# Performance work log

Hardware: AMD Instinct MI355X
Metric: run time of the kernel (lower is better)

Reference implementation:

```python
import jax, jax.numpy as jnp
import numpy as np

HIDDEN = 2048
INPUT = 2048
BATCH = 4096


def setup_inputs() -> dict:
    key = jax.random.key(0)
    ks = jax.random.split(key, 7)
    x = jax.random.normal(ks[0], (BATCH, INPUT), dtype=jnp.float32)
    h = jax.random.normal(ks[1], (BATCH, HIDDEN), dtype=jnp.float32)
    c = jax.random.normal(ks[2], (BATCH, HIDDEN), dtype=jnp.float32)
    # learned parameters (RandomNormal init stddev=0.05 analogue; scale irrelevant for correctness)
    w_ih = jax.random.normal(ks[3], (4, INPUT, HIDDEN), dtype=jnp.float32) * 0.05
    w_hh = jax.random.normal(ks[4], (4, HIDDEN, HIDDEN), dtype=jnp.float32) * 0.05
    b_ih = jax.random.normal(ks[5], (4, HIDDEN), dtype=jnp.float32) * 0.05
    b_hh = jax.random.normal(ks[6], (4, HIDDEN), dtype=jnp.float32) * 0.05
    return {"x": x, "h": h, "c": c, "w_ih": w_ih, "w_hh": w_hh, "b_ih": b_ih, "b_hh": b_hh}


def reference(x, h, c, w_ih, w_hh, b_ih, b_hh):
    # gates: [4, B, H] = x @ w_ih[g] and h @ w_hh[g], batched over gate dim g
    gates = (
        jnp.einsum("bi,gih->gbh", x, w_ih)
        + jnp.einsum("bh,ghk->gbk", h, w_hh)
        + (b_ih + b_hh)[:, None, :]
    )
    ingate = jax.nn.sigmoid(gates[0])
    forgetgate = jax.nn.sigmoid(gates[1])
    cellgate = jnp.tanh(gates[2])
    outgate = jax.nn.sigmoid(gates[3])
    c_new = forgetgate * c + ingate * cellgate
    h_new = outgate * jnp.tanh(c_new)
    return (h_new, c_new)
```

## Files before the change

kernel.cpp:

```cpp
#include <hip/hip_runtime.h>

#define BATCH  4096
#define HIDDEN 2048
#define INPUT  2048
#define KDIM   4096
#define NDIM   8192

#define BM 128
#define BN 128
#define BK 32

typedef __attribute__((ext_vector_type(8))) short short8;
typedef __attribute__((ext_vector_type(4))) float float4v;


__device__ __forceinline__ unsigned short f2bf(float f) {
    union { float f; unsigned u; } v; v.f = f;
    unsigned r = v.u + 0x7FFFu + ((v.u >> 16) & 1u);
    return (unsigned short)(r >> 16);
}

__device__ __forceinline__ void gl2lds16(const unsigned short* g, unsigned short* l) {
    __builtin_amdgcn_global_load_lds(
        (const __attribute__((address_space(1))) unsigned int*)g,
        (__attribute__((address_space(3))) unsigned int*)l,
        16, 0, 0);
}

__device__ __forceinline__ float sigm(float x) {
    return 1.0f / (1.0f + __expf(-x));
}
__device__ __forceinline__ float tanh_fast(float x) {
    return 2.0f / (1.0f + __expf(-2.0f * x)) - 1.0f;
}


__global__ void pack_x_kernel(const float* __restrict__ x, const float* __restrict__ h,
                              unsigned short* __restrict__ Xb) {
    int idx = blockIdx.x * 256 + threadIdx.x;
    int b  = idx >> 9;
    int ko = idx & 511;
    const float* src = (ko < 256) ? (x + (size_t)b * INPUT  + (size_t)ko * 8)
                                  : (h + (size_t)b * HIDDEN + (size_t)(ko - 256) * 8);
    float4 v0 = *(const float4*)(src);
    float4 v1 = *(const float4*)(src + 4);
    union { unsigned short us[8]; uint4 v; } o;
    o.us[0] = f2bf(v0.x); o.us[1] = f2bf(v0.y); o.us[2] = f2bf(v0.z); o.us[3] = f2bf(v0.w);
    o.us[4] = f2bf(v1.x); o.us[5] = f2bf(v1.y); o.us[6] = f2bf(v1.z); o.us[7] = f2bf(v1.w);
    *(uint4*)(Xb + (size_t)b * KDIM + (size_t)ko * 8) = o.v;
}


__global__ void pack_w_kernel(const float* __restrict__ w_ih, const float* __restrict__ w_hh,
                              unsigned short* __restrict__ Wt) {
    __shared__ float tile[64][33];
    int k0 = blockIdx.x * 64;
    int n0 = blockIdx.y * 32;
    int g  = n0 >> 11;
    int j0 = n0 & 2047;
    const float* src = (k0 < INPUT)
        ? (w_ih + (size_t)g * INPUT  * HIDDEN + (size_t)k0 * HIDDEN + j0)
        : (w_hh + (size_t)g * HIDDEN * HIDDEN + (size_t)(k0 - INPUT) * HIDDEN + j0);

    int tcol = threadIdx.x & 31;
    int trow = threadIdx.x >> 5;
#pragma unroll
    for (int p = 0; p < 8; ++p)
        tile[trow + p * 8][tcol] = src[(size_t)(trow + p * 8) * HIDDEN + tcol];
    __syncthreads();

    int tk = threadIdx.x & 63;
    int tn = threadIdx.x >> 6;
#pragma unroll
    for (int p = 0; p < 8; ++p)
        Wt[(size_t)(n0 + tn + p * 4) * KDIM + k0 + tk] = f2bf(tile[tk][tn + p * 4]);
}


__global__ __launch_bounds__(256, 2)
void gemm_kernel(const unsigned short* __restrict__ A,
                 const unsigned short* __restrict__ B,
                 float* __restrict__ C) {
    __shared__ unsigned short As[BM * BK];
    __shared__ unsigned short Bs[BN * BK];

    const int tid  = threadIdx.x;
    const int m0   = blockIdx.y * BM;
    const int n0   = blockIdx.x * BN;
    const int wave = tid >> 6;
    const int lane = tid & 63;
    const int ln   = lane & 15;
    const int kq   = lane >> 4;
    const int wm   = (wave >> 1) * 64;
    const int wn   = (wave & 1) * 64;

    const int s0 = tid, s1 = tid + 256;
    const unsigned short* gA0 = A + (size_t)(m0 + (s0 >> 2)) * KDIM + (s0 & 3) * 8;
    const unsigned short* gA1 = A + (size_t)(m0 + (s1 >> 2)) * KDIM + (s1 & 3) * 8;
    const unsigned short* gB0 = B + (size_t)(n0 + (s0 >> 2)) * KDIM + (s0 & 3) * 8;
    const unsigned short* gB1 = B + (size_t)(n0 + (s1 >> 2)) * KDIM + (s1 & 3) * 8;
    unsigned short* lA0 = As + s0 * 8;
    unsigned short* lA1 = As + s1 * 8;
    unsigned short* lB0 = Bs + s0 * 8;
    unsigned short* lB1 = Bs + s1 * 8;

    float4v acc[4][4];
#pragma unroll
    for (int i = 0; i < 4; ++i)
#pragma unroll
        for (int j = 0; j < 4; ++j)
            acc[i][j] = (float4v){0.f, 0.f, 0.f, 0.f};

    const int a_off = (wm + ln) * BK + kq * 8;
    const int b_off = (wn + ln) * BK + kq * 8;

    for (int kt = 0; kt < KDIM / BK; ++kt) {
        const int ko = kt * BK;
        gl2lds16(gA0 + ko, lA0);
        gl2lds16(gA1 + ko, lA1);
        gl2lds16(gB0 + ko, lB0);
        gl2lds16(gB1 + ko, lB1);
        __syncthreads();

        short8 af[4], bf[4];
#pragma unroll
        for (int mi = 0; mi < 4; ++mi)
            af[mi] = *(const short8*)(As + a_off + mi * 16 * BK);
#pragma unroll
        for (int ni = 0; ni < 4; ++ni)
            bf[ni] = *(const short8*)(Bs + b_off + ni * 16 * BK);

#pragma unroll
        for (int mi = 0; mi < 4; ++mi)
#pragma unroll
            for (int ni = 0; ni < 4; ++ni)
                acc[mi][ni] = __builtin_amdgcn_mfma_f32_16x16x32_bf16(
                    af[mi], bf[ni], acc[mi][ni], 0, 0, 0);

        __syncthreads();
    }

#pragma unroll
    for (int mi = 0; mi < 4; ++mi) {
#pragma unroll
        for (int ni = 0; ni < 4; ++ni) {
            int col  = n0 + wn + ni * 16 + ln;
            int rowb = m0 + wm + mi * 16 + kq * 4;
#pragma unroll
            for (int j = 0; j < 4; ++j)
                C[(size_t)(rowb + j) * NDIM + col] = acc[mi][ni][j];
        }
    }
}


__global__ void lstm_epilogue_kernel(const float* __restrict__ Cg, const float* __restrict__ c,
                                     const float* __restrict__ b_ih, const float* __restrict__ b_hh,
                                     float* __restrict__ out) {
    int idx = blockIdx.x * 256 + threadIdx.x;
    int b = idx >> 9;
    int j = (idx & 511) * 4;

    const float* row = Cg + (size_t)b * NDIM;
    float4 g0 = *(const float4*)(row + j);
    float4 g1 = *(const float4*)(row + HIDDEN + j);
    float4 g2 = *(const float4*)(row + 2 * HIDDEN + j);
    float4 g3 = *(const float4*)(row + 3 * HIDDEN + j);

    float4 bi0 = *(const float4*)(b_ih + j);
    float4 bi1 = *(const float4*)(b_ih + HIDDEN + j);
    float4 bi2 = *(const float4*)(b_ih + 2 * HIDDEN + j);
    float4 bi3 = *(const float4*)(b_ih + 3 * HIDDEN + j);
    float4 bh0 = *(const float4*)(b_hh + j);
    float4 bh1 = *(const float4*)(b_hh + HIDDEN + j);
    float4 bh2 = *(const float4*)(b_hh + 2 * HIDDEN + j);
    float4 bh3 = *(const float4*)(b_hh + 3 * HIDDEN + j);

    float4 cv = *(const float4*)(c + (size_t)b * HIDDEN + j);

    float4 hn, cn;
    {
        float ig = sigm(g0.x + bi0.x + bh0.x);
        float fg = sigm(g1.x + bi1.x + bh1.x);
        float cg = tanh_fast(g2.x + bi2.x + bh2.x);
        float og = sigm(g3.x + bi3.x + bh3.x);
        cn.x = fg * cv.x + ig * cg;
        hn.x = og * tanh_fast(cn.x);
    }
    {
        float ig = sigm(g0.y + bi0.y + bh0.y);
        float fg = sigm(g1.y + bi1.y + bh1.y);
        float cg = tanh_fast(g2.y + bi2.y + bh2.y);
        float og = sigm(g3.y + bi3.y + bh3.y);
        cn.y = fg * cv.y + ig * cg;
        hn.y = og * tanh_fast(cn.y);
    }
    {
        float ig = sigm(g0.z + bi0.z + bh0.z);
        float fg = sigm(g1.z + bi1.z + bh1.z);
        float cg = tanh_fast(g2.z + bi2.z + bh2.z);
        float og = sigm(g3.z + bi3.z + bh3.z);
        cn.z = fg * cv.z + ig * cg;
        hn.z = og * tanh_fast(cn.z);
    }
    {
        float ig = sigm(g0.w + bi0.w + bh0.w);
        float fg = sigm(g1.w + bi1.w + bh1.w);
        float cg = tanh_fast(g2.w + bi2.w + bh2.w);
        float og = sigm(g3.w + bi3.w + bh3.w);
        cn.w = fg * cv.w + ig * cg;
        hn.w = og * tanh_fast(cn.w);
    }

    size_t o = (size_t)b * HIDDEN + j;
    *(float4*)(out + o) = hn;
    *(float4*)(out + (size_t)BATCH * HIDDEN + o) = cn;
}


extern "C" void kernel_launch(void* const* d_in, const int* in_sizes, int n_in,
                              void* d_out, int out_size, void* d_ws, size_t ws_size,
                              hipStream_t stream) {
    const float* x    = (const float*)d_in[0];
    const float* h    = (const float*)d_in[1];
    const float* c    = (const float*)d_in[2];
    const float* w_ih = (const float*)d_in[3];
    const float* w_hh = (const float*)d_in[4];
    const float* b_ih = (const float*)d_in[5];
    const float* b_hh = (const float*)d_in[6];
    float* out = (float*)d_out;

    const size_t XB_BYTES = (size_t)BATCH * KDIM * 2;
    const size_t WT_BYTES = (size_t)NDIM * KDIM * 2;
    unsigned short* Xb = (unsigned short*)d_ws;
    unsigned short* Wt = (unsigned short*)((char*)d_ws + XB_BYTES);
    float*          Cg = (float*)((char*)d_ws + XB_BYTES + WT_BYTES);

    hipLaunchKernelGGL(pack_x_kernel, dim3((size_t)BATCH * KDIM / 8 / 256), dim3(256), 0, stream,
                       x, h, Xb);
    hipLaunchKernelGGL(pack_w_kernel, dim3(KDIM / 64, NDIM / 32), dim3(256), 0, stream,
                       w_ih, w_hh, Wt);
    hipLaunchKernelGGL(gemm_kernel, dim3(NDIM / BN, BATCH / BM), dim3(256), 0, stream,
                       Xb, Wt, Cg);
    hipLaunchKernelGGL(lstm_epilogue_kernel, dim3((size_t)BATCH * HIDDEN / 4 / 256), dim3(256), 0, stream,
                       Cg, c, b_ih, b_hh, out);
}
```

Before: 590.6 us.

## Interleave gate columns in packed weights and fuse LSTM epilogue into GEMM

The weight pack now interleaves the four gate columns for each hidden unit (column 4*j+g), so each 16-column MFMA tile holds all four gates for four hidden units. The GEMM epilogue uses lane shuffles to bring the four gate values of one (row, hidden) pair into one lane, applies the bias and LSTM nonlinearities, and writes h_new and c_new directly. This removes the 128 MB fp32 gate intermediate write and read-back and one kernel launch. In exchange the output stores are scalar and strided rather than float4, and the epilogue does extra shuffles and per-lane loads of c and bias.

```diff
diff --git a/kernel.cpp b/kernel.cpp
--- a/kernel.cpp
+++ b/kernel.cpp
@@ -5,7 +5,6 @@
 #define INPUT  2048
 #define KDIM   4096
 #define NDIM   8192
-
 #define BM 128
 #define BN 128
 #define BK 32
@@ -72,15 +71,20 @@
     int tk = threadIdx.x & 63;
     int tn = threadIdx.x >> 6;
 #pragma unroll
-    for (int p = 0; p < 8; ++p)
-        Wt[(size_t)(n0 + tn + p * 4) * KDIM + k0 + tk] = f2bf(tile[tk][tn + p * 4]);
+    for (int p = 0; p < 8; ++p) {
+        int j = j0 + tn + p * 4;
+        Wt[(size_t)(4 * j + g) * KDIM + k0 + tk] = f2bf(tile[tk][tn + p * 4]);
+    }
 }
 
 
 __global__ __launch_bounds__(256, 2)
 void gemm_kernel(const unsigned short* __restrict__ A,
                  const unsigned short* __restrict__ B,
-                 float* __restrict__ C) {
+                 const float* __restrict__ c,
+                 const float* __restrict__ b_ih,
+                 const float* __restrict__ b_hh,
+                 float* __restrict__ out) {
     __shared__ unsigned short As[BM * BK];
     __shared__ unsigned short Bs[BN * BK];
 
@@ -122,99 +126,63 @@
         gl2lds16(gB1 + ko, lB1);
         __syncthreads();
 
-        short8 af[4], bf[4];
+        short8 af[4], bfr[4];
 #pragma unroll
         for (int mi = 0; mi < 4; ++mi)
             af[mi] = *(const short8*)(As + a_off + mi * 16 * BK);
 #pragma unroll
         for (int ni = 0; ni < 4; ++ni)
-            bf[ni] = *(const short8*)(Bs + b_off + ni * 16 * BK);
+            bfr[ni] = *(const short8*)(Bs + b_off + ni * 16 * BK);
 
 #pragma unroll
         for (int mi = 0; mi < 4; ++mi)
 #pragma unroll
             for (int ni = 0; ni < 4; ++ni)
                 acc[mi][ni] = __builtin_amdgcn_mfma_f32_16x16x32_bf16(
-                    af[mi], bf[ni], acc[mi][ni], 0, 0, 0);
+                    af[mi], bfr[ni], acc[mi][ni], 0, 0, 0);
 
         __syncthreads();
     }
 
-#pragma unroll
-    for (int mi = 0; mi < 4; ++mi) {
-#pragma unroll
-        for (int ni = 0; ni < 4; ++ni) {
-            int col  = n0 + wn + ni * 16 + ln;
-            int rowb = m0 + wm + mi * 16 + kq * 4;
-#pragma unroll
-            for (int j = 0; j < 4; ++j)
-                C[(size_t)(rowb + j) * NDIM + col] = acc[mi][ni][j];
+    const int q = lane & 3;
+    const int t = (lane & 15) >> 2;
+    const size_t HB = (size_t)BATCH * HIDDEN;
+
+#pragma unroll
+    for (int ni = 0; ni < 4; ++ni) {
+        const int jg = ((n0 + wn + ni * 16) >> 2) + t;
+        const float b0 = b_ih[jg]              + b_hh[jg];
+        const float b1 = b_ih[HIDDEN + jg]     + b_hh[HIDDEN + jg];
+        const float b2 = b_ih[2 * HIDDEN + jg] + b_hh[2 * HIDDEN + jg];
+        const float b3 = b_ih[3 * HIDDEN + jg] + b_hh[3 * HIDDEN + jg];
+#pragma unroll
+        for (int mi = 0; mi < 4; ++mi) {
+            float4v v = acc[mi][ni];
+            float t1 = __shfl_xor((q & 1) ? v[0] : v[1], 1);
+            float t2 = __shfl_xor((q & 1) ? v[2] : v[3], 1);
+            v[0] = (q & 1) ? t1 : v[0];
+            v[1] = (q & 1) ? v[1] : t1;
+            v[2] = (q & 1) ? t2 : v[2];
+            v[3] = (q & 1) ? v[3] : t2;
+            float t3 = __shfl_xor((q & 2) ? v[0] : v[2], 2);
+            float t4 = __shfl_xor((q & 2) ? v[1] : v[3], 2);
+            v[0] = (q & 2) ? t3 : v[0];
+            v[1] = (q & 2) ? t4 : v[1];
+            v[2] = (q & 2) ? v[2] : t3;
+            v[3] = (q & 2) ? v[3] : t4;
+
+            const int row = m0 + wm + mi * 16 + kq * 4 + q;
+            const float ig = sigm(v[0] + b0);
+            const float fg = sigm(v[1] + b1);
+            const float cg = tanh_fast(v[2] + b2);
+            const float og = sigm(v[3] + b3);
+            const float cv = c[(size_t)row * HIDDEN + jg];
+            const float cn = fg * cv + ig * cg;
+            const float hn = og * tanh_fast(cn);
+            out[(size_t)row * HIDDEN + jg] = hn;
+            out[HB + (size_t)row * HIDDEN + jg] = cn;
         }
     }
-}
-
-
-__global__ void lstm_epilogue_kernel(const float* __restrict__ Cg, const float* __restrict__ c,
-                                     const float* __restrict__ b_ih, const float* __restrict__ b_hh,
-                                     float* __restrict__ out) {
-    int idx = blockIdx.x * 256 + threadIdx.x;
-    int b = idx >> 9;
-    int j = (idx & 511) * 4;
-
-    const float* row = Cg + (size_t)b * NDIM;
-    float4 g0 = *(const float4*)(row + j);
-    float4 g1 = *(const float4*)(row + HIDDEN + j);
-    float4 g2 = *(const float4*)(row + 2 * HIDDEN + j);
-    float4 g3 = *(const float4*)(row + 3 * HIDDEN + j);
-
-    float4 bi0 = *(const float4*)(b_ih + j);
-    float4 bi1 = *(const float4*)(b_ih + HIDDEN + j);
-    float4 bi2 = *(const float4*)(b_ih + 2 * HIDDEN + j);
-    float4 bi3 = *(const float4*)(b_ih + 3 * HIDDEN + j);
-    float4 bh0 = *(const float4*)(b_hh + j);
-    float4 bh1 = *(const float4*)(b_hh + HIDDEN + j);
-    float4 bh2 = *(const float4*)(b_hh + 2 * HIDDEN + j);
-    float4 bh3 = *(const float4*)(b_hh + 3 * HIDDEN + j);
-
-    float4 cv = *(const float4*)(c + (size_t)b * HIDDEN + j);
-
-    float4 hn, cn;
-    {
-        float ig = sigm(g0.x + bi0.x + bh0.x);
-        float fg = sigm(g1.x + bi1.x + bh1.x);
-        float cg = tanh_fast(g2.x + bi2.x + bh2.x);
-        float og = sigm(g3.x + bi3.x + bh3.x);
-        cn.x = fg * cv.x + ig * cg;
-        hn.x = og * tanh_fast(cn.x);
-    }
-    {
-        float ig = sigm(g0.y + bi0.y + bh0.y);
-        float fg = sigm(g1.y + bi1.y + bh1.y);
-        float cg = tanh_fast(g2.y + bi2.y + bh2.y);
-        float og = sigm(g3.y + bi3.y + bh3.y);
-        cn.y = fg * cv.y + ig * cg;
-        hn.y = og * tanh_fast(cn.y);
-    }
-    {
-        float ig = sigm(g0.z + bi0.z + bh0.z);
-        float fg = sigm(g1.z + bi1.z + bh1.z);
-        float cg = tanh_fast(g2.z + bi2.z + bh2.z);
-        float og = sigm(g3.z + bi3.z + bh3.z);
-        cn.z = fg * cv.z + ig * cg;
-        hn.z = og * tanh_fast(cn.z);
-    }
-    {
-        float ig = sigm(g0.w + bi0.w + bh0.w);
-        float fg = sigm(g1.w + bi1.w + bh1.w);
-        float cg = tanh_fast(g2.w + bi2.w + bh2.w);
-        float og = sigm(g3.w + bi3.w + bh3.w);
-        cn.w = fg * cv.w + ig * cg;
-        hn.w = og * tanh_fast(cn.w);
-    }
-
-    size_t o = (size_t)b * HIDDEN + j;
-    *(float4*)(out + o) = hn;
-    *(float4*)(out + (size_t)BATCH * HIDDEN + o) = cn;
 }
 
 
@@ -231,17 +199,13 @@
     float* out = (float*)d_out;
 
     const size_t XB_BYTES = (size_t)BATCH * KDIM * 2;
-    const size_t WT_BYTES = (size_t)NDIM * KDIM * 2;
     unsigned short* Xb = (unsigned short*)d_ws;
     unsigned short* Wt = (unsigned short*)((char*)d_ws + XB_BYTES);
-    float*          Cg = (float*)((char*)d_ws + XB_BYTES + WT_BYTES);
 
     hipLaunchKernelGGL(pack_x_kernel, dim3((size_t)BATCH * KDIM / 8 / 256), dim3(256), 0, stream,
                        x, h, Xb);
     hipLaunchKernelGGL(pack_w_kernel, dim3(KDIM / 64, NDIM / 32), dim3(256), 0, stream,
                        w_ih, w_hh, Wt);
     hipLaunchKernelGGL(gemm_kernel, dim3(NDIM / BN, BATCH / BM), dim3(256), 0, stream,
-                       Xb, Wt, Cg);
-    hipLaunchKernelGGL(lstm_epilogue_kernel, dim3((size_t)BATCH * HIDDEN / 4 / 256), dim3(256), 0, stream,
-                       Cg, c, b_ih, b_hh, out);
-}
+                       Xb, Wt, c, b_ih, b_hh, out);
+}
```

New measurement: 565.0 us. -4.3%, faster.
